# Optimization experiments

Hardware: AMD Instinct MI355X
Metric: run time of the kernel (lower is better)

The kernel has to match this reference:

```python
import jax, jax.numpy as jnp
import numpy as np

K_MASK = -2.3819763e+38
NUM_HEADS = 16
NUM_KV_HEADS = 8
FEATURES = 2048
HEAD_DIM = 128
WINDOW = 1024
SOFT_CAP = 50.0
B, T = 2, 2048


def apply_rope(inputs, positions, head_dim, max_wavelength=10000):
    # inputs: [B, T, N, H], positions: [B, T]
    fraction = 2 * jnp.arange(0, head_dim // 2) / head_dim
    timescale = max_wavelength ** fraction
    sinusoid_inp = positions[..., None] / timescale[None, None, :]  # [B,T,H/2]
    sinusoid_inp = sinusoid_inp[..., None, :]  # [B,T,1,H/2]
    sin = jnp.sin(sinusoid_inp)
    cos = jnp.cos(sinusoid_inp)
    first_half, second_half = jnp.split(inputs, 2, axis=-1)
    first_part = first_half * cos - second_half * sin
    second_part = second_half * cos + first_half * sin
    return jnp.concatenate([first_part, second_part], axis=-1).astype(inputs.dtype)


def setup_inputs() -> dict:
    key = jax.random.key(0)
    k1, k2, k3, k4 = jax.random.split(key, 4)
    std = 0.02
    x = jax.random.normal(k1, (B, T, FEATURES), dtype=jnp.float32)
    segment_pos = jnp.broadcast_to(jnp.arange(T, dtype=jnp.int32), (B, T))
    # causal prefill mask [B, T, T]
    attn_mask = jnp.broadcast_to(jnp.tril(jnp.ones((T, T), dtype=bool)), (B, T, T))
    wq = jax.random.normal(k2, (NUM_HEADS, FEATURES, HEAD_DIM), dtype=jnp.float32) * std
    wkv = jax.random.normal(k3, (2, NUM_KV_HEADS, FEATURES, HEAD_DIM), dtype=jnp.float32) * std
    wo = jax.random.normal(k4, (NUM_HEADS, HEAD_DIM, FEATURES), dtype=jnp.float32) * std
    return {"x": x, "segment_pos": segment_pos, "attn_mask": attn_mask,
            "wq": wq, "wkv": wkv, "wo": wo}


def reference(x, segment_pos, attn_mask, wq, wkv, wo):
    # Projections (GQA path: num_kv_heads != num_heads)
    q = jnp.einsum('BTD,NDH->BTNH', x, wq)              # [B,T,N,H]
    k = jnp.einsum('BSD,KDH->BSKH', x, wkv[0])          # [B,S,K,H]
    v = jnp.einsum('BSD,KDH->BSKH', x, wkv[1])          # [B,S,K,H]

    q = apply_rope(q, segment_pos, HEAD_DIM)
    q = q * HEAD_DIM ** (-0.5)
    k = apply_rope(k, segment_pos, HEAD_DIM)

    b, t, n, h = q.shape
    g = n // NUM_KV_HEADS
    qg = q.reshape(b, t, NUM_KV_HEADS, g, h)
    logits = jnp.einsum('BTKGH,BSKH->BTKGS', qg, k)
    s = logits.shape[-1]
    logits = logits.reshape(b, t, n, s)

    # soft cap
    logits = jnp.tanh(logits / SOFT_CAP) * SOFT_CAP

    # sliding-window mask combined with attn_mask
    cache_positions = jnp.arange(s)[None, None, :]
    sp = segment_pos[:, :, None]
    sliding_mask = (cache_positions >= sp - WINDOW + 1) & (cache_positions <= sp + WINDOW - 1)
    mask = sliding_mask & attn_mask  # [B,T,S]

    padded_logits = jnp.where(mask[:, :, None, :], logits, K_MASK)
    probs = jax.nn.softmax(padded_logits, axis=-1).astype(k.dtype)

    pg = probs.reshape(b, t, NUM_KV_HEADS, g, s)
    encoded = jnp.einsum('BTKGS,BSKH->BTKGH', pg, v).reshape(b, t, n, h)
    attn_output = jnp.einsum('BTNH,NHD->BTD', encoded, wo)
    return attn_output
```

## Files before the change

### kernel.cpp

```cpp
#include <hip/hip_runtime.h>

typedef unsigned short u16;
typedef unsigned int u32;
typedef __attribute__((ext_vector_type(8))) short bfx8;
typedef __attribute__((ext_vector_type(4))) float fx4;

static __device__ __forceinline__ float b2f(u16 u) {
    union { float f; u32 i; } c; c.i = ((u32)u) << 16; return c.f;
}
static __device__ __forceinline__ u16 f2b(float f) {
    union { float f; u32 i; } c; c.f = f;
    u32 r = c.i + 0x7FFFu + ((c.i >> 16) & 1u);
    return (u16)(r >> 16);
}
typedef const __attribute__((address_space(1))) unsigned int* gas1;
typedef __attribute__((address_space(3))) unsigned int* las3;
static __device__ __forceinline__ void gll16(const void* g, void* l) {
    __builtin_amdgcn_global_load_lds((gas1)g, (las3)l, 16, 0, 0);
}

__global__ __launch_bounds__(256) void k_prep1(const float* __restrict__ x, u16* __restrict__ xb,
                                               const float* __restrict__ wq, const float* __restrict__ wkv,
                                               u16* __restrict__ wb1) {
    __shared__ float t[128 * 33];
    int bid = blockIdx.x, tid = threadIdx.x;
    if (bid < 4096) {
        size_t i = ((size_t)bid * 256 + tid) * 8;
        float4 a = *(const float4*)(x + i);
        float4 b = *(const float4*)(x + i + 4);
        union { u16 e[8]; uint4 v; } o;
        o.e[0] = f2b(a.x); o.e[1] = f2b(a.y); o.e[2] = f2b(a.z); o.e[3] = f2b(a.w);
        o.e[4] = f2b(b.x); o.e[5] = f2b(b.y); o.e[6] = f2b(b.z); o.e[7] = f2b(b.w);
        *(uint4*)(xb + i) = o.v;
        return;
    }
    int idx = bid - 4096;
    int ci = idx & 31;
    int k0 = (idx >> 5) << 5;
    int c0 = ci << 7;
    const float* src;
    if (ci < 16)      src = wq  + (size_t)ci * 2048 * 128;
    else if (ci < 24) src = wkv + (size_t)(ci - 16) * 2048 * 128;
    else              src = wkv + (size_t)(8 + ci - 24) * 2048 * 128;
#pragma unroll
    for (int i = 0; i < 16; i++) {
        int id2 = i * 256 + tid;
        int kk = id2 >> 7, cc = id2 & 127;
        t[cc * 33 + kk] = src[(size_t)(k0 + kk) * 128 + cc];
    }
    __syncthreads();
#pragma unroll
    for (int i = 0; i < 16; i++) {
        int id2 = i * 256 + tid;
        int cc = id2 >> 5, kk = id2 & 31;
        wb1[(size_t)(c0 + cc) * 2048 + k0 + kk] = f2b(t[cc * 33 + kk]);
    }
}

template <int BM, int OUT_BF16>
__global__ __launch_bounds__(512, 2) void k_gemmdw(const u16* __restrict__ A, const u16* __restrict__ Bt,
                                                   void* __restrict__ C, int M, int N, int K) {
    constexpr int MF = BM / 32;
    constexpr int MH = MF / 2;
    constexpr int AF = BM / 8;
    constexpr int FR = AF + 32;
    constexpr int LPW = FR / 8;
    constexpr int C0 = (4 * MH + 16) / 8;
    constexpr int C2 = MH / 2;
    __shared__ u16 lds[2 * FR * 512];

    int tid = threadIdx.x, wave = tid >> 6, lane = tid & 63;
    int quad = lane >> 4, l16 = lane & 15;
    int wm = wave >> 2, wn = wave & 3;

    int nwg = gridDim.x * gridDim.y;
    int bid = blockIdx.y * gridDim.x + blockIdx.x;
    int swz = (bid & 7) * (nwg >> 3) + (bid >> 3);
    int bx = swz % gridDim.x, by = swz / gridDim.x;
    int r0 = by * BM, c0 = bx << 8;

    fx4 zero = {0.f, 0.f, 0.f, 0.f};
    fx4 acc[MF][4];
#pragma unroll
    for (int m = 0; m < MF; m++)
#pragma unroll
        for (int n = 0; n < 4; n++) acc[m][n] = zero;

    const u16* gsrc[LPW];
    int lof[LPW];
#pragma unroll
    for (int j = 0; j < LPW; j++) {
        int isA, fi;
        if (j < C0) {
            int idx = wave * C0 + j;
            if (idx < 4 * MH) {
                int g = idx / (2 * MH), r = idx % (2 * MH);
                isA = 1; fi = ((g * MF + (r >> 1)) << 1) + (r & 1);
            } else {
                int t = idx - 4 * MH;
                int cg = ((t >> 2) << 2) + ((t >> 1) & 1);
                isA = 0; fi = (cg << 1) + (t & 1);
            }
        } else if (j < C0 + 2) {
            int t = wave * 2 + (j - C0);
            int cg = ((t >> 2) << 2) + 2 + ((t >> 1) & 1);
            isA = 0; fi = (cg << 1) + (t & 1);
        } else {
            int idx = wave * C2 + (j - C0 - 2);
            int g = idx / (2 * MH), r = idx % (2 * MH);
            isA = 1; fi = ((g * MF + MH + (r >> 1)) << 1) + (r & 1);
        }
        gsrc[j] = (isA ? A + (size_t)(r0 + (fi >> 1) * 16 + l16) * K
                       : Bt + (size_t)(c0 + (fi >> 1) * 16 + l16) * K) + (fi & 1) * 32 + quad * 8;
        lof[j] = (isA ? fi : AF + fi) * 512;
    }

    int NT = K >> 6;
#pragma unroll
    for (int j = 0; j < LPW; j++) gll16(gsrc[j], lds + lof[j]);

    bfx8 ax[MH][2], bu[2][2], bv[2][2];
#define PH(vm) asm volatile("s_waitcnt vmcnt(%0)" : : "n"(vm) : "memory"); __builtin_amdgcn_s_barrier();
#define RD_A(h) _Pragma("unroll") for (int m = 0; m < MH; m++) _Pragma("unroll") for (int kk = 0; kk < 2; kk++) \
        ax[m][kk] = *(const bfx8*)(buf + (((wm * MF + (h) * MH + m) << 1) + kk) * 512 + lane * 8);
#define RD_B(dst, pair) _Pragma("unroll") for (int n = 0; n < 2; n++) _Pragma("unroll") for (int kk = 0; kk < 2; kk++) \
        dst[n][kk] = *(const bfx8*)(buf + (AF + (((wn << 2) + (pair) * 2 + n) << 1) + kk) * 512 + lane * 8);
#define MM(h, pair, B) __builtin_amdgcn_s_setprio(1);                                                      \
    _Pragma("unroll") for (int kk = 0; kk < 2; kk++) _Pragma("unroll") for (int m = 0; m < MH; m++)        \
    _Pragma("unroll") for (int n = 0; n < 2; n++)                                                          \
        acc[(h) * MH + m][(pair) * 2 + n] =                                                                \
            __builtin_amdgcn_mfma_f32_16x16x32_bf16(ax[m][kk], B[n][kk], acc[(h) * MH + m][(pair) * 2 + n], 0, 0, 0); \
    __builtin_amdgcn_s_setprio(0);

    for (int T = 0; T < NT - 1; ++T) {
        const u16* buf = lds + (T & 1) * (FR * 512);
        u16* nb = lds + ((T + 1) & 1) * (FR * 512);
        size_t go = (size_t)(T + 1) * 64;
#pragma unroll
        for (int j = 0; j < C0; j++) gll16(gsrc[j] + go, nb + lof[j]);
        PH(LPW)
        RD_A(0) RD_B(bu, 0)
        MM(0, 0, bu)
#pragma unroll
        for (int j = C0; j < C0 + 2; j++) gll16(gsrc[j] + go, nb + lof[j]);
        PH(LPW)
        RD_B(bv, 1)
        MM(0, 1, bv)
#pragma unroll
        for (int j = C0 + 2; j < LPW; j++) gll16(gsrc[j] + go, nb + lof[j]);
        PH(LPW)
        RD_A(1)
        MM(1, 0, bu)
        MM(1, 1, bv)
    }
    {
        const u16* buf = lds + ((NT - 1) & 1) * (FR * 512);
        PH(LPW - C0)
        RD_A(0) RD_B(bu, 0)
        MM(0, 0, bu)
        PH(C2)
        RD_B(bv, 1)
        MM(0, 1, bv)
        PH(0)
        RD_A(1)
        MM(1, 0, bu)
        MM(1, 1, bv)
    }
#undef PH
#undef RD_A
#undef RD_B
#undef MM
#pragma unroll
    for (int m = 0; m < MF; m++)
#pragma unroll
        for (int n = 0; n < 4; n++) {
            int col = c0 + wn * 64 + n * 16 + l16;
#pragma unroll
            for (int r = 0; r < 4; r++) {
                int row = r0 + wm * (BM / 2) + m * 16 + quad * 4 + r;
                float v = acc[m][n][r];
                if (OUT_BF16) ((u16*)C)[(size_t)row * N + col] = f2b(v);
                else          ((float*)C)[(size_t)row * N + col] = v;
            }
        }
}

__global__ __launch_bounds__(256) void k_mid(u16* __restrict__ qkv, u16* __restrict__ Kb,
                                             u16* __restrict__ Vt,
                                             const float* __restrict__ wo, u16* __restrict__ wb2) {
    __shared__ __align__(16) char smem[128 * 136 * 2];
    int bid = blockIdx.x, tid = threadIdx.x;
    if (bid < 4096) {
        float* sc = (float*)smem;
        int b = bid >> 11, t = bid & 2047;
        u16* row = qkv + (size_t)bid * 4096;
        float tf = (float)t;
        const float RS = 0.08838834764831845f;
        const float LT = 0.20762050593046f;
        if (tid < 64) {
            float ang = tf * exp2f(-LT * (float)tid);
            float s, c; sincosf(ang, &s, &c);
            sc[tid] = s; sc[tid + 64] = c;
        }
        __syncthreads();
#pragma unroll
        for (int i = 0; i < 4; i++) {
            int idx = tid + i * 256;
            int n = idx >> 6, hp = idx & 63;
            float x1 = b2f(row[n * 128 + hp]);
            float x2 = b2f(row[n * 128 + hp + 64]);
            float s = sc[hp], c = sc[hp + 64];
            row[n * 128 + hp]      = f2b((x1 * c - x2 * s) * RS);
            row[n * 128 + hp + 64] = f2b((x2 * c + x1 * s) * RS);
        }
#pragma unroll
        for (int i = 0; i < 2; i++) {
            int idx = tid + i * 256;
            int kh = idx >> 6, hp = idx & 63;
            float x1 = b2f(row[2048 + kh * 128 + hp]);
            float x2 = b2f(row[2048 + kh * 128 + hp + 64]);
            float s = sc[hp], c = sc[hp + 64];
            size_t o = ((size_t)(b * 8 + kh) * 2048 + t) * 128 + hp;
            Kb[o]      = f2b(x1 * c - x2 * s);
            Kb[o + 64] = f2b(x2 * c + x1 * s);
        }
        return;
    }
    if (bid < 4352) {
        u16* t = (u16*)smem;
        int idx = bid - 4096;
        int bk = idx >> 4;
        int t0 = (idx & 15) << 7;
        const u16* src = qkv + ((size_t)((bk >> 3) * 2048 + t0)) * 4096 + 3072 + (bk & 7) * 128;
        u16* dst = Vt + (size_t)bk * 128 * 2048 + t0;
#pragma unroll
        for (int it = 0; it < 8; it++) {
            int ch = tid + it * 256;
            int tt = ch >> 4, c8 = (ch & 15) << 3;
            *(uint4*)(t + tt * 136 + c8) = *(const uint4*)(src + (size_t)tt * 4096 + c8);
        }
        __syncthreads();
#pragma unroll
        for (int it = 0; it < 8; it++) {
            int ch = tid + it * 256;
            int h = ch >> 4, s8 = (ch & 15) << 3;
            union { uint4 v; u16 e[8]; } vv;
#pragma unroll
            for (int j = 0; j < 8; j++) vv.e[j] = t[(s8 + j) * 136 + h];
            *(uint4*)(dst + (size_t)h * 2048 + s8) = vv.v;
        }
        return;
    }
    float* t = (float*)smem;
    int idx = bid - 4352;
    int c0 = (idx & 15) << 7;
    int k0 = (idx >> 4) << 5;
#pragma unroll
    for (int i = 0; i < 16; i++) {
        int id2 = i * 256 + tid;
        int kk = id2 >> 7, cc = id2 & 127;
        t[cc * 33 + kk] = wo[(size_t)(k0 + kk) * 2048 + c0 + cc];
    }
    __syncthreads();
#pragma unroll
    for (int i = 0; i < 16; i++) {
        int id2 = i * 256 + tid;
        int cc = id2 >> 5, kk = id2 & 31;
        wb2[(size_t)(c0 + cc) * 2048 + k0 + kk] = f2b(t[cc * 33 + kk]);
    }
}

__global__ __launch_bounds__(512, 4) void k_attn(const u16* __restrict__ qkv, const u16* __restrict__ Kb,
                                                 const u16* __restrict__ Vt, u16* __restrict__ enc) {
    __shared__ u16 Ks[2][16 * 512];
    __shared__ u16 Vs[2][16 * 512];
    __shared__ u16 Pl[8 * 1024];
    int t0 = blockIdx.x << 6;
    int kh = blockIdx.y, b = blockIdx.z;
    int tid = threadIdx.x, wave = tid >> 6, lane = tid & 63;
    int quad = lane >> 4, l16 = lane & 15;
    int n = (kh << 1) + (wave >> 2);
    int tw = t0 + ((wave & 3) << 4);
    const u16* Qp = qkv + (size_t)b * 2048 * 4096 + n * 128;
    const u16* Kp = Kb + (size_t)(b * 8 + kh) * 2048 * 128;
    const u16* Vp = Vt + (size_t)(b * 8 + kh) * 128 * 2048;

    bfx8 aq[4];
#pragma unroll
    for (int kb = 0; kb < 4; kb++)
        aq[kb] = *(const bfx8*)(Qp + (size_t)(tw + l16) * 4096 + kb * 32 + quad * 8);

    const u16* kgp[2]; const u16* vgp[2];
#pragma unroll
    for (int q = 0; q < 2; q++) {
        int f = wave * 2 + q;
        kgp[q] = Kp + (size_t)((f >> 2) * 16 + l16) * 128 + (f & 3) * 32 + quad * 8;
        vgp[q] = Vp + (size_t)((f >> 1) * 16 + l16) * 2048 + (f & 1) * 32 + quad * 8;
    }
    u16* Pw = Pl + wave * 1024;

    fx4 zero = {0.f, 0.f, 0.f, 0.f};
    fx4 o_acc[8];
#pragma unroll
    for (int hb = 0; hb < 8; hb++) o_acc[hb] = zero;
    float lsum[4] = {0.f, 0.f, 0.f, 0.f};

    const float C1 = 0.057707801635559f;
    const float C2 = 144.269504088896f;

    int s_lo = t0 - 1023; if (s_lo < 0) s_lo = 0;
    int ts0 = s_lo >> 6, ts1 = t0 >> 6;

#pragma unroll
    for (int q = 0; q < 2; q++) {
        int f = wave * 2 + q;
        gll16(kgp[q] + (size_t)(ts0 << 6) * 128, Ks[0] + f * 512);
        gll16(vgp[q] + (ts0 << 6), Vs[0] + f * 512);
    }

    for (int ts = ts0; ts <= ts1; ts++) {
        int cur = (ts - ts0) & 1;
        int s0 = ts << 6;
        __builtin_amdgcn_s_barrier();
        if (ts < ts1) {
            int s1 = (ts + 1) << 6;
#pragma unroll
            for (int q = 0; q < 2; q++) {
                int f = wave * 2 + q;
                gll16(kgp[q] + (size_t)s1 * 128, Ks[cur ^ 1] + f * 512);
                gll16(vgp[q] + s1, Vs[cur ^ 1] + f * 512);
            }
            asm volatile("s_waitcnt vmcnt(4)" : : : "memory");
        } else {
            asm volatile("s_waitcnt vmcnt(0)" : : : "memory");
        }
        __builtin_amdgcn_s_barrier();

        if (s0 <= tw + 15 && s0 + 63 >= tw - 1023) {
            const u16* Kc = Ks[cur];
            const u16* Vc = Vs[cur];
            bool full = (s0 + 63 <= tw) && (s0 >= tw - 1008);
            if (full) {
#pragma unroll
                for (int nb = 0; nb < 4; nb++) {
                    fx4 sacc = zero;
                    __builtin_amdgcn_s_setprio(1);
#pragma unroll
                    for (int kb = 0; kb < 4; kb++) {
                        bfx8 bk = *(const bfx8*)(Kc + (nb * 4 + kb) * 512 + lane * 8);
                        sacc = __builtin_amdgcn_mfma_f32_16x16x32_bf16(aq[kb], bk, sacc, 0, 0, 0);
                    }
                    __builtin_amdgcn_s_setprio(0);
                    int base0 = ((nb >> 1) * 64 + ((nb & 1) * 2 + (l16 >> 3)) * 16 + quad * 4) * 8 + (l16 & 7);
#pragma unroll
                    for (int r = 0; r < 4; r++) {
                        float u = __builtin_amdgcn_exp2f(sacc[r] * C1);
                        float p = __builtin_amdgcn_exp2f(-C2 * __builtin_amdgcn_rcpf(u + 1.f));
                        lsum[r] += p;
                        Pw[base0 + r * 8] = f2b(p);
                    }
                }
            } else {
#pragma unroll
                for (int nb = 0; nb < 4; nb++) {
                    int sb = s0 + (nb << 4);
                    int base0 = ((nb >> 1) * 64 + ((nb & 1) * 2 + (l16 >> 3)) * 16 + quad * 4) * 8 + (l16 & 7);
                    if (sb <= tw + 15 && sb + 15 >= tw - 1023) {
                        fx4 sacc = zero;
#pragma unroll
                        for (int kb = 0; kb < 4; kb++) {
                            bfx8 bk = *(const bfx8*)(Kc + (nb * 4 + kb) * 512 + lane * 8);
                            sacc = __builtin_amdgcn_mfma_f32_16x16x32_bf16(aq[kb], bk, sacc, 0, 0, 0);
                        }
                        int sg = sb + l16;
#pragma unroll
                        for (int r = 0; r < 4; r++) {
                            int tg = tw + quad * 4 + r;
                            float u = __builtin_amdgcn_exp2f(sacc[r] * C1);
                            float p = __builtin_amdgcn_exp2f(-C2 * __builtin_amdgcn_rcpf(u + 1.f));
                            p = (sg <= tg && sg >= tg - 1023) ? p : 0.f;
                            lsum[r] += p;
                            Pw[base0 + r * 8] = f2b(p);
                        }
                    } else {
#pragma unroll
                        for (int r = 0; r < 4; r++) Pw[base0 + r * 8] = 0;
                    }
                }
            }
            asm volatile("s_waitcnt lgkmcnt(0)" : : : "memory");
            __builtin_amdgcn_sched_barrier(0);
            bfx8 pf[2];
#pragma unroll
            for (int kk = 0; kk < 2; kk++)
                pf[kk] = *(const bfx8*)(Pw + kk * 512 + lane * 8);
            __builtin_amdgcn_s_setprio(1);
#pragma unroll
            for (int hb = 0; hb < 8; hb++)
#pragma unroll
                for (int kk = 0; kk < 2; kk++) {
                    bfx8 vf = *(const bfx8*)(Vc + (hb * 2 + kk) * 512 + lane * 8);
                    o_acc[hb] = __builtin_amdgcn_mfma_f32_16x16x32_bf16(pf[kk], vf, o_acc[hb], 0, 0, 0);
                }
            __builtin_amdgcn_s_setprio(0);
        }
    }
#pragma unroll
    for (int r = 0; r < 4; r++) {
#pragma unroll
        for (int off = 1; off < 16; off <<= 1)
            lsum[r] += __shfl_xor(lsum[r], off);
        lsum[r] = 1.0f / lsum[r];
    }
#pragma unroll
    for (int hb = 0; hb < 8; hb++) {
        int h = hb * 16 + l16;
#pragma unroll
        for (int r = 0; r < 4; r++) {
            int tg = tw + quad * 4 + r;
            enc[((size_t)(b * 2048 + tg) * 16 + n) * 128 + h] = f2b(o_acc[hb][r] * lsum[r]);
        }
    }
}

extern "C" void kernel_launch(void* const* d_in, const int* in_sizes, int n_in,
                              void* d_out, int out_size, void* d_ws, size_t ws_size,
                              hipStream_t stream) {
    const float* x   = (const float*)d_in[0];
    const float* wq  = (const float*)d_in[3];
    const float* wkv = (const float*)d_in[4];
    const float* wo  = (const float*)d_in[5];
    char* ws = (char*)d_ws;
    const size_t MiB = 1024 * 1024;
    u16* xb  = (u16*)(ws);
    u16* wb1 = (u16*)(ws + 16 * MiB);
    u16* qkv = (u16*)(ws + 32 * MiB);
    u16* Kb  = (u16*)(ws);
    u16* wb2 = (u16*)(ws + 8 * MiB);
    u16* enc = (u16*)(ws + 16 * MiB);
    u16* Vt  = (u16*)d_out;

    k_prep1<<<6144, 256, 0, stream>>>(x, xb, wq, wkv, wb1);
    k_gemmdw<256, 1><<<dim3(16, 16), 512, 0, stream>>>(xb, wb1, qkv, 4096, 4096, 2048);
    k_mid<<<5376, 256, 0, stream>>>(qkv, Kb, Vt, wo, wb2);
    k_attn<<<dim3(32, 8, 2), 512, 0, stream>>>(qkv, Kb, Vt, enc);
    k_gemmdw<128, 0><<<dim3(8, 32), 512, 0, stream>>>(enc, wb2, d_out, 4096, 2048, 2048);
}
```

Before: 345.3 us.

## Merge GEMM load phases into two barriers and write Q head-major

The GEMM main loop goes from three wait/barrier phases per k-step to two. It issues A and both B pairs' loads together, reads all B fragments up front, and adds an explicit barrier before the second half's MFMAs to keep LDS reuse safe. Separately, the RoPE pass now writes rotated Q into a contiguous per-head buffer in the output region instead of back into the strided qkv rows, so attention loads Q with a 128-element stride rather than 4096. The risk is less load/compute interleaving in the GEMM, plus more B registers live at once.

```diff
diff --git a/kernel.cpp b/kernel.cpp
--- a/kernel.cpp
+++ b/kernel.cpp
@@ -66,7 +66,7 @@
     constexpr int FR = AF + 32;
     constexpr int LPW = FR / 8;
     constexpr int C0 = (4 * MH + 16) / 8;
-    constexpr int C2 = MH / 2;
+    constexpr int C2 = LPW - C0 - 2;
     __shared__ u16 lds[2 * FR * 512];
 
     int tid = threadIdx.x, wave = tid >> 6, lane = tid & 63;
@@ -137,32 +137,28 @@
         u16* nb = lds + ((T + 1) & 1) * (FR * 512);
         size_t go = (size_t)(T + 1) * 64;
 #pragma unroll
-        for (int j = 0; j < C0; j++) gll16(gsrc[j] + go, nb + lof[j]);
+        for (int j = 0; j < C0 + 2; j++) gll16(gsrc[j] + go, nb + lof[j]);
         PH(LPW)
-        RD_A(0) RD_B(bu, 0)
+        RD_A(0) RD_B(bu, 0) RD_B(bv, 1)
         MM(0, 0, bu)
-#pragma unroll
-        for (int j = C0; j < C0 + 2; j++) gll16(gsrc[j] + go, nb + lof[j]);
-        PH(LPW)
-        RD_B(bv, 1)
-        MM(0, 1, bv)
 #pragma unroll
         for (int j = C0 + 2; j < LPW; j++) gll16(gsrc[j] + go, nb + lof[j]);
         PH(LPW)
+        MM(0, 1, bv)
         RD_A(1)
+        __builtin_amdgcn_s_barrier();
         MM(1, 0, bu)
         MM(1, 1, bv)
     }
     {
         const u16* buf = lds + ((NT - 1) & 1) * (FR * 512);
-        PH(LPW - C0)
-        RD_A(0) RD_B(bu, 0)
+        PH(C2)
+        RD_A(0) RD_B(bu, 0) RD_B(bv, 1)
         MM(0, 0, bu)
-        PH(C2)
-        RD_B(bv, 1)
+        PH(0)
         MM(0, 1, bv)
-        PH(0)
         RD_A(1)
+        __builtin_amdgcn_s_barrier();
         MM(1, 0, bu)
         MM(1, 1, bv)
     }
@@ -185,15 +181,15 @@
         }
 }
 
-__global__ __launch_bounds__(256) void k_mid(u16* __restrict__ qkv, u16* __restrict__ Kb,
-                                             u16* __restrict__ Vt,
+__global__ __launch_bounds__(256) void k_mid(const u16* __restrict__ qkv, u16* __restrict__ Qb,
+                                             u16* __restrict__ Kb, u16* __restrict__ Vt,
                                              const float* __restrict__ wo, u16* __restrict__ wb2) {
     __shared__ __align__(16) char smem[128 * 136 * 2];
     int bid = blockIdx.x, tid = threadIdx.x;
     if (bid < 4096) {
         float* sc = (float*)smem;
         int b = bid >> 11, t = bid & 2047;
-        u16* row = qkv + (size_t)bid * 4096;
+        const u16* row = qkv + (size_t)bid * 4096;
         float tf = (float)t;
         const float RS = 0.08838834764831845f;
         const float LT = 0.20762050593046f;
@@ -210,8 +206,9 @@
             float x1 = b2f(row[n * 128 + hp]);
             float x2 = b2f(row[n * 128 + hp + 64]);
             float s = sc[hp], c = sc[hp + 64];
-            row[n * 128 + hp]      = f2b((x1 * c - x2 * s) * RS);
-            row[n * 128 + hp + 64] = f2b((x2 * c + x1 * s) * RS);
+            size_t o = ((size_t)(b * 16 + n) * 2048 + t) * 128 + hp;
+            Qb[o]      = f2b((x1 * c - x2 * s) * RS);
+            Qb[o + 64] = f2b((x2 * c + x1 * s) * RS);
         }
 #pragma unroll
         for (int i = 0; i < 2; i++) {
@@ -270,7 +267,7 @@
     }
 }
 
-__global__ __launch_bounds__(512, 4) void k_attn(const u16* __restrict__ qkv, const u16* __restrict__ Kb,
+__global__ __launch_bounds__(512, 4) void k_attn(const u16* __restrict__ Qb, const u16* __restrict__ Kb,
                                                  const u16* __restrict__ Vt, u16* __restrict__ enc) {
     __shared__ u16 Ks[2][16 * 512];
     __shared__ u16 Vs[2][16 * 512];
@@ -281,14 +278,14 @@
     int quad = lane >> 4, l16 = lane & 15;
     int n = (kh << 1) + (wave >> 2);
     int tw = t0 + ((wave & 3) << 4);
-    const u16* Qp = qkv + (size_t)b * 2048 * 4096 + n * 128;
+    const u16* Qp = Qb + (size_t)(b * 16 + n) * 2048 * 128;
     const u16* Kp = Kb + (size_t)(b * 8 + kh) * 2048 * 128;
     const u16* Vp = Vt + (size_t)(b * 8 + kh) * 128 * 2048;
 
     bfx8 aq[4];
 #pragma unroll
     for (int kb = 0; kb < 4; kb++)
-        aq[kb] = *(const bfx8*)(Qp + (size_t)(tw + l16) * 4096 + kb * 32 + quad * 8);
+        aq[kb] = *(const bfx8*)(Qp + (size_t)(tw + l16) * 128 + kb * 32 + quad * 8);
 
     const u16* kgp[2]; const u16* vgp[2];
 #pragma unroll
@@ -439,10 +436,11 @@
     u16* wb2 = (u16*)(ws + 8 * MiB);
     u16* enc = (u16*)(ws + 16 * MiB);
     u16* Vt  = (u16*)d_out;
+    u16* Qb  = (u16*)((char*)d_out + 8 * MiB);
 
     k_prep1<<<6144, 256, 0, stream>>>(x, xb, wq, wkv, wb1);
     k_gemmdw<256, 1><<<dim3(16, 16), 512, 0, stream>>>(xb, wb1, qkv, 4096, 4096, 2048);
-    k_mid<<<5376, 256, 0, stream>>>(qkv, Kb, Vt, wo, wb2);
-    k_attn<<<dim3(32, 8, 2), 512, 0, stream>>>(qkv, Kb, Vt, enc);
+    k_mid<<<5376, 256, 0, stream>>>(qkv, Qb, Kb, Vt, wo, wb2);
+    k_attn<<<dim3(32, 8, 2), 512, 0, stream>>>(Qb, Kb, Vt, enc);
     k_gemmdw<128, 0><<<dim3(8, 32), 512, 0, stream>>>(enc, wb2, d_out, 4096, 2048, 2048);
 }
```

After: 338.0 us. 1.02x faster.
